# Optimization experiments

Hardware: AMD Instinct MI355X
Metric: run time of the kernel (lower is better)

Reference implementation:

```python
import jax, jax.numpy as jnp
import numpy as np

N_NODES = 50000

def _gat_layer(x, src, dst, W, a_l, a_r, bias, alpha, agg, act, n_nodes):
    # x: [N, in]; W: [in, H*F]; a_l, a_r: [H, F]; bias: [H*F]
    H, F = a_l.shape
    z = (x @ W).reshape(n_nodes, H, F)                      # [N,H,F]
    el = jnp.einsum('nhf,hf->nh', z, a_l)                   # [N,H]
    er = jnp.einsum('nhf,hf->nh', z, a_r)                   # [N,H]
    e = jax.nn.leaky_relu(el[src] + er[dst], alpha)         # [E,H]
    # segment softmax over in-edges of each destination node
    m = jax.ops.segment_max(e, dst, num_segments=n_nodes)   # [N,H]
    ex = jnp.exp(e - m[dst])                                # [E,H]
    s = jax.ops.segment_sum(ex, dst, num_segments=n_nodes)  # [N,H]
    attn = ex / jnp.maximum(s[dst], 1e-9)                   # [E,H]
    msg = attn[:, :, None] * z[src]                         # [E,H,F]
    h = jax.ops.segment_sum(msg, dst, num_segments=n_nodes) # [N,H,F]
    # identity residual (in_feats == H*F) as in DGL GATConv
    h = h + x.reshape(n_nodes, -1, F)
    h = h + bias.reshape(1, H, F)
    if agg == 'flatten':
        h = h.reshape(n_nodes, H * F)
    else:  # mean over heads
        h = h.mean(axis=1)
    if act is not None:
        h = act(h)
    return h


def setup_inputs() -> dict:
    key = jax.random.key(0)
    ks = jax.random.split(key, 14)
    N, E, D = N_NODES, 800000, 128
    H, F = 4, 32
    sc_in = 1.0 / np.sqrt(D)
    sc_h = 1.0 / np.sqrt(H * F)
    inp = {
        'feats': jax.random.normal(ks[0], (N, D), jnp.float32),
        'src': jax.random.randint(ks[1], (E,), 0, N),
        'dst': jax.random.randint(ks[2], (E,), 0, N),
        'W1': jax.random.normal(ks[3], (D, H * F), jnp.float32) * sc_in,
        'al1': jax.random.normal(ks[4], (H, F), jnp.float32) * sc_h,
        'ar1': jax.random.normal(ks[5], (H, F), jnp.float32) * sc_h,
        'b1': jnp.zeros((H * F,), jnp.float32),
        'W2': jax.random.normal(ks[6], (H * F, H * F), jnp.float32) * sc_h,
        'al2': jax.random.normal(ks[7], (H, F), jnp.float32) * sc_h,
        'ar2': jax.random.normal(ks[8], (H, F), jnp.float32) * sc_h,
        'b2': jnp.zeros((H * F,), jnp.float32),
        'Wp': jax.random.normal(ks[9], (F, 1), jnp.float32) / np.sqrt(F),
        'bp': jnp.zeros((1,), jnp.float32),
    }
    return inp


def reference(feats, src, dst, W1, al1, ar1, b1, W2, al2, ar2, b2, Wp, bp):
    h = _gat_layer(feats, src, dst, W1, al1, ar1, b1, 0.2, 'flatten', jax.nn.elu, N_NODES)
    h = _gat_layer(h, src, dst, W2, al2, ar2, b2, 0.2, 'mean', None, N_NODES)
    return h @ Wp + bp  # [N, 1]
```

## Files before the change

kernel.cpp:

```cpp
#include <hip/hip_runtime.h>
#include <hip/hip_bf16.h>

#define NN 50000
#define NE 800000
#define HF 128
#define MAXDEG 64

#define OFF_FLAG   0u
#define OFF_FX     3801088u
#define OFF_WC1    16601088u
#define OFF_WC2    16633856u
#define OFF_PAR    16666624u
#define OFF_Z      16668672u
#define OFF_H1     29468672u
#define OFF_EL     42268672u
#define OFF_ER     43068672u
#define OFF_FILL   54000128u
#define OFF_ADJ2   60000000u

typedef __hip_bfloat16 bf16;
typedef unsigned short us16;

#define PREP_RANK_B   3125
#define PREP_FEATS_B  6250
#define PREP_SMALL_B  132
#define PREP_GRID     (PREP_RANK_B + PREP_FEATS_B + PREP_SMALL_B)
#define GEMM_B 782

typedef __attribute__((ext_vector_type(8))) short bf16x8;
typedef __attribute__((ext_vector_type(4))) float f32x4;

__device__ __forceinline__ float us2f(us16 u) {
  union { unsigned int i; float f; } c; c.i = ((unsigned int)u) << 16; return c.f;
}
__device__ __forceinline__ us16 f2us(float f) {
  bf16 h = __float2bfloat16(f);
  union { bf16 h; us16 u; } c; c.h = h; return c.u;
}
__device__ __forceinline__ float blo(unsigned v) {
  union { unsigned i; float f; } c; c.i = v << 16; return c.f;
}
__device__ __forceinline__ float bhi(unsigned v) {
  union { unsigned i; float f; } c; c.i = v & 0xffff0000u; return c.f;
}
__device__ __forceinline__ unsigned pk2(float a, float b) {
  return (unsigned)f2us(a) | ((unsigned)f2us(b) << 16);
}

__device__ __forceinline__ int detect_f32(const us16* __restrict__ u) {
  int t = threadIdx.x;
  int mx = 0;
  for (int i = t; i < 2048; i += 256) {
    int e = (u[i] >> 7) & 0xFF;
    mx = mx > e ? mx : e;
  }
#pragma unroll
  for (int m = 32; m >= 1; m >>= 1) {
    int o = __shfl_xor(mx, m);
    mx = mx > o ? mx : o;
  }
  __shared__ int sred[4];
  if ((t & 63) == 0) sred[t >> 6] = mx;
  __syncthreads();
  int a = sred[0] > sred[1] ? sred[0] : sred[1];
  int b = sred[2] > sred[3] ? sred[2] : sred[3];
  int r = a > b ? a : b;
  return r >= 135;
}

__global__ __launch_bounds__(256) void k_prep(
    const void* __restrict__ feats, us16* __restrict__ fx,
    const void* s0, const void* s1, const void* s2, const void* s3, const void* s4,
    const void* s5, const void* s6, const void* s7, const void* s8, const void* s9,
    us16* d0, us16* d1, us16* d2, us16* d3, us16* d4,
    us16* d5, us16* d6, us16* d7, us16* d8, us16* d9,
    const int* __restrict__ src, const int* __restrict__ dst,
    int* __restrict__ fill, int* __restrict__ adj2, int* __restrict__ flag) {
  int b = blockIdx.x;
  if (b < PREP_RANK_B) {
    int e = b * 256 + threadIdx.x;
    if (e < NE) {
      int d = dst[e];
      int r = atomicAdd(&fill[d], 1);
      if (r < MAXDEG) adj2[(d << 6) + r] = src[e];
    }
    return;
  }
  int f = detect_f32((const us16*)s0);
  if (b == PREP_RANK_B && threadIdx.x == 0) *flag = f;
  if (b < PREP_RANK_B + PREP_FEATS_B) {
    int i = ((b - PREP_RANK_B) * 256 + threadIdx.x) * 4;
    if (f) {
      float4 v = *(const float4*)((const float*)feats + i);
      ushort4 o;
      o.x = f2us(v.x); o.y = f2us(v.y); o.z = f2us(v.z); o.w = f2us(v.w);
      *(ushort4*)(fx + i) = o;
    } else {
      *(ushort4*)(fx + i) = *(const ushort4*)((const us16*)feats + i);
    }
  } else {
    const void* sp[10] = {s0, s1, s2, s3, s4, s5, s6, s7, s8, s9};
    us16* dp[10] = {d0, d1, d2, d3, d4, d5, d6, d7, d8, d9};
    const int cnt[10] = {16384, 16384, 128, 128, 128, 128, 128, 128, 32, 1};
    int gid = (b - PREP_RANK_B - PREP_FEATS_B) * 256 + threadIdx.x;
    int base = 0;
#pragma unroll
    for (int p = 0; p < 10; ++p) {
      int loc = gid - base;
      if (loc >= 0 && loc < cnt[p])
        dp[p][loc] = f ? f2us(((const float*)sp[p])[loc]) : ((const us16*)sp[p])[loc];
      base += cnt[p];
    }
  }
}

__global__ __launch_bounds__(256) void k_gemm(const us16* __restrict__ X,
                                              const us16* __restrict__ W,
                                              us16* __restrict__ Z,
                                              const us16* __restrict__ al,
                                              const us16* __restrict__ ar,
                                              float* __restrict__ el,
                                              float* __restrict__ er) {
  __shared__ us16 Wl[HF * HF];
  int tid = threadIdx.x;
  for (int e = tid; e < HF * HF; e += 256) {
    int k = e >> 7, n = e & 127;
    int d = ((((k >> 5) * 8 + (n >> 4)) * 4 + ((k >> 3) & 3)) * 16 + (n & 15)) * 8 + (k & 7);
    Wl[d] = W[e];
  }
  __syncthreads();

  int w = tid >> 6;
  int lane = tid & 63;
  int q = lane >> 4;
  int c = lane & 15;
  int m0 = blockIdx.x * 64 + w * 16;

  int rA = m0 + c;
  if (rA >= NN) rA = NN - 1;
  const us16* xrow = X + (size_t)rA * HF;

  f32x4 acc[8] = {};
#pragma unroll
  for (int s = 0; s < 4; ++s) {
    bf16x8 a = *(const bf16x8*)&xrow[s * 32 + q * 8];
#pragma unroll
    for (int t = 0; t < 8; ++t) {
      bf16x8 bb = *(const bf16x8*)&Wl[((((s * 8) + t) * 4 + q) * 16 + c) * 8];
      acc[t] = __builtin_amdgcn_mfma_f32_16x16x32_bf16(a, bb, acc[t], 0, 0, 0);
    }
  }

#pragma unroll
  for (int reg = 0; reg < 4; ++reg) {
    int row = m0 + q * 4 + reg;
    if (row < NN) {
      us16* zrow = Z + (size_t)row * HF;
#pragma unroll
      for (int t = 0; t < 8; ++t) zrow[t * 16 + c] = f2us(acc[t][reg]);
    }
  }

  float alv[8], arv[8];
#pragma unroll
  for (int t = 0; t < 8; ++t) {
    alv[t] = us2f(al[t * 16 + c]);
    arv[t] = us2f(ar[t * 16 + c]);
  }
#pragma unroll
  for (int reg = 0; reg < 4; ++reg) {
    int row = m0 + q * 4 + reg;
    float pl[4], pr[4];
#pragma unroll
    for (int h = 0; h < 4; ++h) {
      pl[h] = acc[2 * h][reg] * alv[2 * h] + acc[2 * h + 1][reg] * alv[2 * h + 1];
      pr[h] = acc[2 * h][reg] * arv[2 * h] + acc[2 * h + 1][reg] * arv[2 * h + 1];
    }
#pragma unroll
    for (int m = 1; m < 16; m <<= 1) {
#pragma unroll
      for (int h = 0; h < 4; ++h) {
        pl[h] += __shfl_xor(pl[h], m);
        pr[h] += __shfl_xor(pr[h], m);
      }
    }
    if (row < NN) {
      int cc = c & 3;
      float vl = cc == 0 ? pl[0] : cc == 1 ? pl[1] : cc == 2 ? pl[2] : pl[3];
      float vr = cc == 0 ? pr[0] : cc == 1 ? pr[1] : cc == 2 ? pr[2] : pr[3];
      if (c < 4) el[row * 4 + cc] = vl;
      else if (c < 8) er[row * 4 + cc] = vr;
    }
  }
}

template <int LAYER>
__global__ __launch_bounds__(256) void k_agg(
    const us16* __restrict__ Z, const float* __restrict__ el,
    const float* __restrict__ er, const int* __restrict__ fill,
    const int* __restrict__ adj2, const us16* __restrict__ resid,
    const us16* __restrict__ bias, us16* __restrict__ Hout,
    const us16* __restrict__ Wp, const us16* __restrict__ bp,
    void* __restrict__ out, const int* __restrict__ flag) {
  int n = blockIdx.x * 4 + (threadIdx.x >> 6);
  int lane = threadIdx.x & 63;
  int g = lane >> 4;
  int p = lane & 15;
  int hl = p >> 2;
  int f0 = p * 8;
  int deg = fill[n];
  if (deg > MAXDEG) deg = MAXDEG;
  int begin = n << 6;
  float erh = er[n * 4 + hl];

  float acc[8] = {};
  float ssum = 0.f;
  int i = g;
  for (; i + 4 < deg; i += 8) {
    int s0 = adj2[begin + i];
    int s1 = adj2[begin + i + 4];
    float l0 = el[s0 * 4 + hl];
    float l1 = el[s1 * 4 + hl];
    uint4 za = *(const uint4*)&Z[(size_t)s0 * HF + f0];
    uint4 zb = *(const uint4*)&Z[(size_t)s1 * HF + f0];
    float sc0 = l0 + erh; sc0 = sc0 > 0.f ? sc0 : 0.2f * sc0;
    float sc1 = l1 + erh; sc1 = sc1 > 0.f ? sc1 : 0.2f * sc1;
    float ex0 = __expf(sc0);
    float ex1 = __expf(sc1);
    ssum += ex0 + ex1;
    acc[0] = fmaf(ex0, blo(za.x), acc[0]); acc[1] = fmaf(ex0, bhi(za.x), acc[1]);
    acc[2] = fmaf(ex0, blo(za.y), acc[2]); acc[3] = fmaf(ex0, bhi(za.y), acc[3]);
    acc[4] = fmaf(ex0, blo(za.z), acc[4]); acc[5] = fmaf(ex0, bhi(za.z), acc[5]);
    acc[6] = fmaf(ex0, blo(za.w), acc[6]); acc[7] = fmaf(ex0, bhi(za.w), acc[7]);
    acc[0] = fmaf(ex1, blo(zb.x), acc[0]); acc[1] = fmaf(ex1, bhi(zb.x), acc[1]);
    acc[2] = fmaf(ex1, blo(zb.y), acc[2]); acc[3] = fmaf(ex1, bhi(zb.y), acc[3]);
    acc[4] = fmaf(ex1, blo(zb.z), acc[4]); acc[5] = fmaf(ex1, bhi(zb.z), acc[5]);
    acc[6] = fmaf(ex1, blo(zb.w), acc[6]); acc[7] = fmaf(ex1, bhi(zb.w), acc[7]);
  }
  if (i < deg) {
    int s = adj2[begin + i];
    float sc = el[s * 4 + hl] + erh;
    sc = sc > 0.f ? sc : 0.2f * sc;
    float ex = __expf(sc);
    ssum += ex;
    uint4 zq = *(const uint4*)&Z[(size_t)s * HF + f0];
    acc[0] = fmaf(ex, blo(zq.x), acc[0]); acc[1] = fmaf(ex, bhi(zq.x), acc[1]);
    acc[2] = fmaf(ex, blo(zq.y), acc[2]); acc[3] = fmaf(ex, bhi(zq.y), acc[3]);
    acc[4] = fmaf(ex, blo(zq.z), acc[4]); acc[5] = fmaf(ex, bhi(zq.z), acc[5]);
    acc[6] = fmaf(ex, blo(zq.w), acc[6]); acc[7] = fmaf(ex, bhi(zq.w), acc[7]);
  }
  ssum += __shfl_xor(ssum, 16); ssum += __shfl_xor(ssum, 32);
#pragma unroll
  for (int j = 0; j < 8; ++j) {
    acc[j] += __shfl_xor(acc[j], 16);
    acc[j] += __shfl_xor(acc[j], 32);
  }
  float inv = 1.f / fmaxf(ssum, 1e-9f);

  uint4 xq = *(const uint4*)&resid[(size_t)n * HF + f0];
  uint4 bq = *(const uint4*)&bias[f0];
  float t0 = fmaf(acc[0], inv, blo(xq.x) + blo(bq.x));
  float t1 = fmaf(acc[1], inv, bhi(xq.x) + bhi(bq.x));
  float t2 = fmaf(acc[2], inv, blo(xq.y) + blo(bq.y));
  float t3 = fmaf(acc[3], inv, bhi(xq.y) + bhi(bq.y));
  float t4 = fmaf(acc[4], inv, blo(xq.z) + blo(bq.z));
  float t5 = fmaf(acc[5], inv, bhi(xq.z) + bhi(bq.z));
  float t6 = fmaf(acc[6], inv, blo(xq.w) + blo(bq.w));
  float t7 = fmaf(acc[7], inv, bhi(xq.w) + bhi(bq.w));

  if (LAYER == 1) {
    t0 = t0 > 0.f ? t0 : __expf(t0) - 1.f;
    t1 = t1 > 0.f ? t1 : __expf(t1) - 1.f;
    t2 = t2 > 0.f ? t2 : __expf(t2) - 1.f;
    t3 = t3 > 0.f ? t3 : __expf(t3) - 1.f;
    t4 = t4 > 0.f ? t4 : __expf(t4) - 1.f;
    t5 = t5 > 0.f ? t5 : __expf(t5) - 1.f;
    t6 = t6 > 0.f ? t6 : __expf(t6) - 1.f;
    t7 = t7 > 0.f ? t7 : __expf(t7) - 1.f;
    if (g == 0) {
      uint4 o;
      o.x = pk2(t0, t1); o.y = pk2(t2, t3); o.z = pk2(t4, t5); o.w = pk2(t6, t7);
      *(uint4*)&Hout[(size_t)n * HF + f0] = o;
    }
  } else {
    t0 += __shfl_xor(t0, 4); t0 += __shfl_xor(t0, 8);
    t1 += __shfl_xor(t1, 4); t1 += __shfl_xor(t1, 8);
    t2 += __shfl_xor(t2, 4); t2 += __shfl_xor(t2, 8);
    t3 += __shfl_xor(t3, 4); t3 += __shfl_xor(t3, 8);
    t4 += __shfl_xor(t4, 4); t4 += __shfl_xor(t4, 8);
    t5 += __shfl_xor(t5, 4); t5 += __shfl_xor(t5, 8);
    t6 += __shfl_xor(t6, 4); t6 += __shfl_xor(t6, 8);
    t7 += __shfl_xor(t7, 4); t7 += __shfl_xor(t7, 8);
    int fw = (p & 3) * 8;
    float pr = 0.25f * (t0 * us2f(Wp[fw]) + t1 * us2f(Wp[fw + 1]) +
                        t2 * us2f(Wp[fw + 2]) + t3 * us2f(Wp[fw + 3]) +
                        t4 * us2f(Wp[fw + 4]) + t5 * us2f(Wp[fw + 5]) +
                        t6 * us2f(Wp[fw + 6]) + t7 * us2f(Wp[fw + 7]));
    pr += __shfl_xor(pr, 1); pr += __shfl_xor(pr, 2);
    if (lane == 0) {
      float res = pr + us2f(bp[0]);
      if (*flag) ((float*)out)[n] = res;
      else ((us16*)out)[n] = f2us(res);
    }
  }
}

extern "C" void kernel_launch(void* const* d_in, const int* in_sizes, int n_in,
                              void* d_out, int out_size, void* d_ws, size_t ws_size,
                              hipStream_t stream) {
  const int* src = (const int*)d_in[1];
  const int* dst = (const int*)d_in[2];
  char* ws = (char*)d_ws;
  int* flag   = (int*)(ws + OFF_FLAG);
  us16* fx    = (us16*)(ws + OFF_FX);
  us16* wc1   = (us16*)(ws + OFF_WC1);
  us16* wc2   = (us16*)(ws + OFF_WC2);
  us16* al1   = (us16*)(ws + OFF_PAR + 0);
  us16* ar1   = (us16*)(ws + OFF_PAR + 256);
  us16* b1    = (us16*)(ws + OFF_PAR + 512);
  us16* al2   = (us16*)(ws + OFF_PAR + 768);
  us16* ar2   = (us16*)(ws + OFF_PAR + 1024);
  us16* b2    = (us16*)(ws + OFF_PAR + 1280);
  us16* wp    = (us16*)(ws + OFF_PAR + 1536);
  us16* bp    = (us16*)(ws + OFF_PAR + 1792);
  us16* z     = (us16*)(ws + OFF_Z);
  us16* h1    = (us16*)(ws + OFF_H1);
  float* el   = (float*)(ws + OFF_EL);
  float* er   = (float*)(ws + OFF_ER);
  int* fill   = (int*)(ws + OFF_FILL);
  int* adj2   = (int*)(ws + OFF_ADJ2);

  hipMemsetAsync(fill, 0, (size_t)NN * 4, stream);

  hipLaunchKernelGGL(k_prep, dim3(PREP_GRID), dim3(256), 0, stream,
                     d_in[0], fx,
                     d_in[3], d_in[7], d_in[4], d_in[5], d_in[6],
                     d_in[8], d_in[9], d_in[10], d_in[11], d_in[12],
                     wc1, wc2, al1, ar1, b1, al2, ar2, b2, wp, bp,
                     src, dst, fill, adj2, flag);

  hipLaunchKernelGGL(k_gemm, dim3(GEMM_B), dim3(256), 0, stream, fx, wc1, z,
                     al1, ar1, el, er);
  hipLaunchKernelGGL((k_agg<1>), dim3(NN / 4), dim3(256), 0, stream, z, el, er, fill, adj2,
                     fx, b1, h1, (us16*)nullptr, (us16*)nullptr, (void*)nullptr, flag);
  hipLaunchKernelGGL(k_gemm, dim3(GEMM_B), dim3(256), 0, stream, h1, wc2, z,
                     al2, ar2, el, er);
  hipLaunchKernelGGL((k_agg<2>), dim3(NN / 4), dim3(256), 0, stream, z, el, er, fill, adj2,
                     h1, b2, (us16*)nullptr, wp, bp, d_out, flag);
}
```

Baseline: 241.6 us.

## Fuse input conversion and adjacency scatter into layer-1 GEMM kernel

Removes the separate prep kernel that converted features and parameters to bf16 in workspace. The layer-1 GEMM now also hosts the edge-scatter blocks and converts fp32 inputs on the fly, and the aggregation kernels read residual, bias and projection weights directly in their native dtype. This cuts one launch and a full read/write pass over the feature matrix, at the cost of more branching and wider fp32 loads in the GEMM and aggregation kernels.

```diff
diff --git a/kernel.cpp b/kernel.cpp
--- a/kernel.cpp
+++ b/kernel.cpp
@@ -7,10 +7,6 @@
 #define MAXDEG 64
 
 #define OFF_FLAG   0u
-#define OFF_FX     3801088u
-#define OFF_WC1    16601088u
-#define OFF_WC2    16633856u
-#define OFF_PAR    16666624u
 #define OFF_Z      16668672u
 #define OFF_H1     29468672u
 #define OFF_EL     42268672u
@@ -21,10 +17,7 @@
 typedef __hip_bfloat16 bf16;
 typedef unsigned short us16;
 
-#define PREP_RANK_B   3125
-#define PREP_FEATS_B  6250
-#define PREP_SMALL_B  132
-#define PREP_GRID     (PREP_RANK_B + PREP_FEATS_B + PREP_SMALL_B)
+#define SCAT_B 3125
 #define GEMM_B 782
 
 typedef __attribute__((ext_vector_type(8))) short bf16x8;
@@ -68,65 +61,42 @@
   return r >= 135;
 }
 
-__global__ __launch_bounds__(256) void k_prep(
-    const void* __restrict__ feats, us16* __restrict__ fx,
-    const void* s0, const void* s1, const void* s2, const void* s3, const void* s4,
-    const void* s5, const void* s6, const void* s7, const void* s8, const void* s9,
-    us16* d0, us16* d1, us16* d2, us16* d3, us16* d4,
-    us16* d5, us16* d6, us16* d7, us16* d8, us16* d9,
+template <int LAYER>
+__global__ __launch_bounds__(256) void k_gemm(
+    const void* __restrict__ Xv, const void* __restrict__ Wv,
+    const void* __restrict__ alr, const void* __restrict__ arr,
+    us16* __restrict__ Z, float* __restrict__ el, float* __restrict__ er,
     const int* __restrict__ src, const int* __restrict__ dst,
-    int* __restrict__ fill, int* __restrict__ adj2, int* __restrict__ flag) {
-  int b = blockIdx.x;
-  if (b < PREP_RANK_B) {
-    int e = b * 256 + threadIdx.x;
-    if (e < NE) {
+    int* __restrict__ fill, int* __restrict__ adj2, int* __restrict__ flagp) {
+  if (LAYER == 1) {
+    if ((int)blockIdx.x < SCAT_B) {
+      int e = blockIdx.x * 256 + threadIdx.x;
       int d = dst[e];
       int r = atomicAdd(&fill[d], 1);
       if (r < MAXDEG) adj2[(d << 6) + r] = src[e];
-    }
-    return;
-  }
-  int f = detect_f32((const us16*)s0);
-  if (b == PREP_RANK_B && threadIdx.x == 0) *flag = f;
-  if (b < PREP_RANK_B + PREP_FEATS_B) {
-    int i = ((b - PREP_RANK_B) * 256 + threadIdx.x) * 4;
-    if (f) {
-      float4 v = *(const float4*)((const float*)feats + i);
-      ushort4 o;
-      o.x = f2us(v.x); o.y = f2us(v.y); o.z = f2us(v.z); o.w = f2us(v.w);
-      *(ushort4*)(fx + i) = o;
-    } else {
-      *(ushort4*)(fx + i) = *(const ushort4*)((const us16*)feats + i);
-    }
+      return;
+    }
+  }
+  int bx = (LAYER == 1) ? (int)blockIdx.x - SCAT_B : (int)blockIdx.x;
+
+  __shared__ us16 Wl[HF * HF];
+  int f;
+  if (LAYER == 1) {
+    f = detect_f32((const us16*)Wv);
+    if (bx == 0 && threadIdx.x == 0) *flagp = f;
   } else {
-    const void* sp[10] = {s0, s1, s2, s3, s4, s5, s6, s7, s8, s9};
-    us16* dp[10] = {d0, d1, d2, d3, d4, d5, d6, d7, d8, d9};
-    const int cnt[10] = {16384, 16384, 128, 128, 128, 128, 128, 128, 32, 1};
-    int gid = (b - PREP_RANK_B - PREP_FEATS_B) * 256 + threadIdx.x;
-    int base = 0;
-#pragma unroll
-    for (int p = 0; p < 10; ++p) {
-      int loc = gid - base;
-      if (loc >= 0 && loc < cnt[p])
-        dp[p][loc] = f ? f2us(((const float*)sp[p])[loc]) : ((const us16*)sp[p])[loc];
-      base += cnt[p];
-    }
-  }
-}
-
-__global__ __launch_bounds__(256) void k_gemm(const us16* __restrict__ X,
-                                              const us16* __restrict__ W,
-                                              us16* __restrict__ Z,
-                                              const us16* __restrict__ al,
-                                              const us16* __restrict__ ar,
-                                              float* __restrict__ el,
-                                              float* __restrict__ er) {
-  __shared__ us16 Wl[HF * HF];
+    f = *flagp;
+  }
+
   int tid = threadIdx.x;
-  for (int e = tid; e < HF * HF; e += 256) {
-    int k = e >> 7, n = e & 127;
-    int d = ((((k >> 5) * 8 + (n >> 4)) * 4 + ((k >> 3) & 3)) * 16 + (n & 15)) * 8 + (k & 7);
-    Wl[d] = W[e];
+  {
+    const float* Wf = (const float*)Wv;
+    const us16* Wb = (const us16*)Wv;
+    for (int e = tid; e < HF * HF; e += 256) {
+      int k = e >> 7, n = e & 127;
+      int d = ((((k >> 5) * 8 + (n >> 4)) * 4 + ((k >> 3) & 3)) * 16 + (n & 15)) * 8 + (k & 7);
+      Wl[d] = f ? f2us(Wf[e]) : Wb[e];
+    }
   }
   __syncthreads();
 
@@ -134,16 +104,29 @@
   int lane = tid & 63;
   int q = lane >> 4;
   int c = lane & 15;
-  int m0 = blockIdx.x * 64 + w * 16;
+  int m0 = bx * 64 + w * 16;
 
   int rA = m0 + c;
   if (rA >= NN) rA = NN - 1;
-  const us16* xrow = X + (size_t)rA * HF;
+  const us16* xb = (const us16*)Xv + (size_t)rA * HF;
+  const float* xf = (const float*)Xv + (size_t)rA * HF;
 
   f32x4 acc[8] = {};
 #pragma unroll
   for (int s = 0; s < 4; ++s) {
-    bf16x8 a = *(const bf16x8*)&xrow[s * 32 + q * 8];
+    bf16x8 a;
+    if (LAYER == 1 && f) {
+      float4 v0 = *(const float4*)&xf[s * 32 + q * 8];
+      float4 v1 = *(const float4*)&xf[s * 32 + q * 8 + 4];
+      union { us16 u[8]; bf16x8 v; } cv;
+      cv.u[0] = f2us(v0.x); cv.u[1] = f2us(v0.y);
+      cv.u[2] = f2us(v0.z); cv.u[3] = f2us(v0.w);
+      cv.u[4] = f2us(v1.x); cv.u[5] = f2us(v1.y);
+      cv.u[6] = f2us(v1.z); cv.u[7] = f2us(v1.w);
+      a = cv.v;
+    } else {
+      a = *(const bf16x8*)&xb[s * 32 + q * 8];
+    }
 #pragma unroll
     for (int t = 0; t < 8; ++t) {
       bf16x8 bb = *(const bf16x8*)&Wl[((((s * 8) + t) * 4 + q) * 16 + c) * 8];
@@ -162,10 +145,14 @@
   }
 
   float alv[8], arv[8];
-#pragma unroll
-  for (int t = 0; t < 8; ++t) {
-    alv[t] = us2f(al[t * 16 + c]);
-    arv[t] = us2f(ar[t * 16 + c]);
+  {
+    const float* alf = (const float*)alr; const us16* alb = (const us16*)alr;
+    const float* arf = (const float*)arr; const us16* arb = (const us16*)arr;
+#pragma unroll
+    for (int t = 0; t < 8; ++t) {
+      alv[t] = f ? alf[t * 16 + c] : us2f(alb[t * 16 + c]);
+      arv[t] = f ? arf[t * 16 + c] : us2f(arb[t * 16 + c]);
+    }
   }
 #pragma unroll
   for (int reg = 0; reg < 4; ++reg) {
@@ -198,10 +185,11 @@
 __global__ __launch_bounds__(256) void k_agg(
     const us16* __restrict__ Z, const float* __restrict__ el,
     const float* __restrict__ er, const int* __restrict__ fill,
-    const int* __restrict__ adj2, const us16* __restrict__ resid,
-    const us16* __restrict__ bias, us16* __restrict__ Hout,
-    const us16* __restrict__ Wp, const us16* __restrict__ bp,
+    const int* __restrict__ adj2, const void* __restrict__ resid,
+    const void* __restrict__ bias, us16* __restrict__ Hout,
+    const void* __restrict__ Wp, const void* __restrict__ bp,
     void* __restrict__ out, const int* __restrict__ flag) {
+  int f = *flag;
   int n = blockIdx.x * 4 + (threadIdx.x >> 6);
   int lane = threadIdx.x & 63;
   int g = lane >> 4;
@@ -257,16 +245,36 @@
   }
   float inv = 1.f / fmaxf(ssum, 1e-9f);
 
-  uint4 xq = *(const uint4*)&resid[(size_t)n * HF + f0];
-  uint4 bq = *(const uint4*)&bias[f0];
-  float t0 = fmaf(acc[0], inv, blo(xq.x) + blo(bq.x));
-  float t1 = fmaf(acc[1], inv, bhi(xq.x) + bhi(bq.x));
-  float t2 = fmaf(acc[2], inv, blo(xq.y) + blo(bq.y));
-  float t3 = fmaf(acc[3], inv, bhi(xq.y) + bhi(bq.y));
-  float t4 = fmaf(acc[4], inv, blo(xq.z) + blo(bq.z));
-  float t5 = fmaf(acc[5], inv, bhi(xq.z) + bhi(bq.z));
-  float t6 = fmaf(acc[6], inv, blo(xq.w) + blo(bq.w));
-  float t7 = fmaf(acc[7], inv, bhi(xq.w) + bhi(bq.w));
+  float rx[8];
+  if (LAYER == 1 && f) {
+    const float* rf = (const float*)resid + (size_t)n * HF + f0;
+    float4 r0 = *(const float4*)rf;
+    float4 r1 = *(const float4*)(rf + 4);
+    rx[0] = r0.x; rx[1] = r0.y; rx[2] = r0.z; rx[3] = r0.w;
+    rx[4] = r1.x; rx[5] = r1.y; rx[6] = r1.z; rx[7] = r1.w;
+  } else {
+    uint4 xq = *(const uint4*)((const us16*)resid + (size_t)n * HF + f0);
+    rx[0] = blo(xq.x); rx[1] = bhi(xq.x); rx[2] = blo(xq.y); rx[3] = bhi(xq.y);
+    rx[4] = blo(xq.z); rx[5] = bhi(xq.z); rx[6] = blo(xq.w); rx[7] = bhi(xq.w);
+  }
+  float bv[8];
+  if (f) {
+    const float* bf_ = (const float*)bias + f0;
+    bv[0] = bf_[0]; bv[1] = bf_[1]; bv[2] = bf_[2]; bv[3] = bf_[3];
+    bv[4] = bf_[4]; bv[5] = bf_[5]; bv[6] = bf_[6]; bv[7] = bf_[7];
+  } else {
+    uint4 bq = *(const uint4*)((const us16*)bias + f0);
+    bv[0] = blo(bq.x); bv[1] = bhi(bq.x); bv[2] = blo(bq.y); bv[3] = bhi(bq.y);
+    bv[4] = blo(bq.z); bv[5] = bhi(bq.z); bv[6] = blo(bq.w); bv[7] = bhi(bq.w);
+  }
+  float t0 = fmaf(acc[0], inv, rx[0] + bv[0]);
+  float t1 = fmaf(acc[1], inv, rx[1] + bv[1]);
+  float t2 = fmaf(acc[2], inv, rx[2] + bv[2]);
+  float t3 = fmaf(acc[3], inv, rx[3] + bv[3]);
+  float t4 = fmaf(acc[4], inv, rx[4] + bv[4]);
+  float t5 = fmaf(acc[5], inv, rx[5] + bv[5]);
+  float t6 = fmaf(acc[6], inv, rx[6] + bv[6]);
+  float t7 = fmaf(acc[7], inv, rx[7] + bv[7]);
 
   if (LAYER == 1) {
     t0 = t0 > 0.f ? t0 : __expf(t0) - 1.f;
@@ -292,14 +300,25 @@
     t6 += __shfl_xor(t6, 4); t6 += __shfl_xor(t6, 8);
     t7 += __shfl_xor(t7, 4); t7 += __shfl_xor(t7, 8);
     int fw = (p & 3) * 8;
-    float pr = 0.25f * (t0 * us2f(Wp[fw]) + t1 * us2f(Wp[fw + 1]) +
-                        t2 * us2f(Wp[fw + 2]) + t3 * us2f(Wp[fw + 3]) +
-                        t4 * us2f(Wp[fw + 4]) + t5 * us2f(Wp[fw + 5]) +
-                        t6 * us2f(Wp[fw + 6]) + t7 * us2f(Wp[fw + 7]));
+    float wv0, wv1, wv2, wv3, wv4, wv5, wv6, wv7;
+    if (f) {
+      const float* wpf = (const float*)Wp;
+      wv0 = wpf[fw];     wv1 = wpf[fw + 1]; wv2 = wpf[fw + 2]; wv3 = wpf[fw + 3];
+      wv4 = wpf[fw + 4]; wv5 = wpf[fw + 5]; wv6 = wpf[fw + 6]; wv7 = wpf[fw + 7];
+    } else {
+      const us16* wpb = (const us16*)Wp;
+      wv0 = us2f(wpb[fw]);     wv1 = us2f(wpb[fw + 1]);
+      wv2 = us2f(wpb[fw + 2]); wv3 = us2f(wpb[fw + 3]);
+      wv4 = us2f(wpb[fw + 4]); wv5 = us2f(wpb[fw + 5]);
+      wv6 = us2f(wpb[fw + 6]); wv7 = us2f(wpb[fw + 7]);
+    }
+    float pr = 0.25f * (t0 * wv0 + t1 * wv1 + t2 * wv2 + t3 * wv3 +
+                        t4 * wv4 + t5 * wv5 + t6 * wv6 + t7 * wv7);
     pr += __shfl_xor(pr, 1); pr += __shfl_xor(pr, 2);
     if (lane == 0) {
-      float res = pr + us2f(bp[0]);
-      if (*flag) ((float*)out)[n] = res;
+      float bpv = f ? ((const float*)bp)[0] : us2f(((const us16*)bp)[0]);
+      float res = pr + bpv;
+      if (f) ((float*)out)[n] = res;
       else ((us16*)out)[n] = f2us(res);
     }
   }
@@ -312,17 +331,6 @@
   const int* dst = (const int*)d_in[2];
   char* ws = (char*)d_ws;
   int* flag   = (int*)(ws + OFF_FLAG);
-  us16* fx    = (us16*)(ws + OFF_FX);
-  us16* wc1   = (us16*)(ws + OFF_WC1);
-  us16* wc2   = (us16*)(ws + OFF_WC2);
-  us16* al1   = (us16*)(ws + OFF_PAR + 0);
-  us16* ar1   = (us16*)(ws + OFF_PAR + 256);
-  us16* b1    = (us16*)(ws + OFF_PAR + 512);
-  us16* al2   = (us16*)(ws + OFF_PAR + 768);
-  us16* ar2   = (us16*)(ws + OFF_PAR + 1024);
-  us16* b2    = (us16*)(ws + OFF_PAR + 1280);
-  us16* wp    = (us16*)(ws + OFF_PAR + 1536);
-  us16* bp    = (us16*)(ws + OFF_PAR + 1792);
   us16* z     = (us16*)(ws + OFF_Z);
   us16* h1    = (us16*)(ws + OFF_H1);
   float* el   = (float*)(ws + OFF_EL);
@@ -332,19 +340,16 @@
 
   hipMemsetAsync(fill, 0, (size_t)NN * 4, stream);
 
-  hipLaunchKernelGGL(k_prep, dim3(PREP_GRID), dim3(256), 0, stream,
-                     d_in[0], fx,
-                     d_in[3], d_in[7], d_in[4], d_in[5], d_in[6],
-                     d_in[8], d_in[9], d_in[10], d_in[11], d_in[12],
-                     wc1, wc2, al1, ar1, b1, al2, ar2, b2, wp, bp,
+  hipLaunchKernelGGL((k_gemm<1>), dim3(SCAT_B + GEMM_B), dim3(256), 0, stream,
+                     d_in[0], d_in[3], d_in[4], d_in[5], z, el, er,
                      src, dst, fill, adj2, flag);
-
-  hipLaunchKernelGGL(k_gemm, dim3(GEMM_B), dim3(256), 0, stream, fx, wc1, z,
-                     al1, ar1, el, er);
-  hipLaunchKernelGGL((k_agg<1>), dim3(NN / 4), dim3(256), 0, stream, z, el, er, fill, adj2,
-                     fx, b1, h1, (us16*)nullptr, (us16*)nullptr, (void*)nullptr, flag);
-  hipLaunchKernelGGL(k_gemm, dim3(GEMM_B), dim3(256), 0, stream, h1, wc2, z,
-                     al2, ar2, el, er);
-  hipLaunchKernelGGL((k_agg<2>), dim3(NN / 4), dim3(256), 0, stream, z, el, er, fill, adj2,
-                     h1, b2, (us16*)nullptr, wp, bp, d_out, flag);
-}
+  hipLaunchKernelGGL((k_agg<1>), dim3(NN / 4), dim3(256), 0, stream, z, el, er,
+                     fill, adj2, d_in[0], d_in[6], h1,
+                     (const void*)nullptr, (const void*)nullptr, (void*)nullptr, flag);
+  hipLaunchKernelGGL((k_gemm<2>), dim3(GEMM_B), dim3(256), 0, stream,
+                     h1, d_in[7], d_in[8], d_in[9], z, el, er,
+                     src, dst, fill, adj2, flag);
+  hipLaunchKernelGGL((k_agg<2>), dim3(NN / 4), dim3(256), 0, stream, z, el, er,
+                     fill, adj2, h1, d_in[10], (us16*)nullptr,
+                     d_in[11], d_in[12], d_out, flag);
+}
```

Result: slower. 283.0 us (+17.1%).

## Store adjacency as 16-bit indices and pre-swizzle GEMM weights in prep

Applied to the files above, without the earlier changes.

The prep kernel now writes the weight matrices already in the MFMA-friendly swizzled layout. The GEMM kernel therefore drops its per-block LDS staging and __syncthreads and reads B fragments straight from global memory (L2-resident), with A fragments hoisted into registers. Separately, the padded adjacency list is stored as uint16 instead of int32, which halves the index traffic in both aggregation kernels. This relies on node ids fitting in 16 bits (NN=50000), and it trades LDS reuse of the weights for repeated global/L2 loads per wave.

```diff
diff --git a/kernel.cpp b/kernel.cpp
--- a/kernel.cpp
+++ b/kernel.cpp
@@ -75,14 +75,14 @@
     us16* d0, us16* d1, us16* d2, us16* d3, us16* d4,
     us16* d5, us16* d6, us16* d7, us16* d8, us16* d9,
     const int* __restrict__ src, const int* __restrict__ dst,
-    int* __restrict__ fill, int* __restrict__ adj2, int* __restrict__ flag) {
+    int* __restrict__ fill, us16* __restrict__ adj2, int* __restrict__ flag) {
   int b = blockIdx.x;
   if (b < PREP_RANK_B) {
     int e = b * 256 + threadIdx.x;
     if (e < NE) {
       int d = dst[e];
       int r = atomicAdd(&fill[d], 1);
-      if (r < MAXDEG) adj2[(d << 6) + r] = src[e];
+      if (r < MAXDEG) adj2[(d << 6) + r] = (us16)src[e];
     }
     return;
   }
@@ -107,29 +107,29 @@
 #pragma unroll
     for (int p = 0; p < 10; ++p) {
       int loc = gid - base;
-      if (loc >= 0 && loc < cnt[p])
-        dp[p][loc] = f ? f2us(((const float*)sp[p])[loc]) : ((const us16*)sp[p])[loc];
+      if (loc >= 0 && loc < cnt[p]) {
+        us16 v = f ? f2us(((const float*)sp[p])[loc]) : ((const us16*)sp[p])[loc];
+        if (p < 2) {
+          int k = loc >> 7, n = loc & 127;
+          int d = ((((k >> 5) * 8 + (n >> 4)) * 4 + ((k >> 3) & 3)) * 16 + (n & 15)) * 8 + (k & 7);
+          dp[p][d] = v;
+        } else {
+          dp[p][loc] = v;
+        }
+      }
       base += cnt[p];
     }
   }
 }
 
 __global__ __launch_bounds__(256) void k_gemm(const us16* __restrict__ X,
-                                              const us16* __restrict__ W,
+                                              const us16* __restrict__ Wc,
                                               us16* __restrict__ Z,
                                               const us16* __restrict__ al,
                                               const us16* __restrict__ ar,
                                               float* __restrict__ el,
                                               float* __restrict__ er) {
-  __shared__ us16 Wl[HF * HF];
   int tid = threadIdx.x;
-  for (int e = tid; e < HF * HF; e += 256) {
-    int k = e >> 7, n = e & 127;
-    int d = ((((k >> 5) * 8 + (n >> 4)) * 4 + ((k >> 3) & 3)) * 16 + (n & 15)) * 8 + (k & 7);
-    Wl[d] = W[e];
-  }
-  __syncthreads();
-
   int w = tid >> 6;
   int lane = tid & 63;
   int q = lane >> 4;
@@ -140,14 +140,17 @@
   if (rA >= NN) rA = NN - 1;
   const us16* xrow = X + (size_t)rA * HF;
 
+  bf16x8 afr[4];
+#pragma unroll
+  for (int s = 0; s < 4; ++s) afr[s] = *(const bf16x8*)&xrow[s * 32 + q * 8];
+
   f32x4 acc[8] = {};
-#pragma unroll
+#pragma unroll 1
   for (int s = 0; s < 4; ++s) {
-    bf16x8 a = *(const bf16x8*)&xrow[s * 32 + q * 8];
 #pragma unroll
     for (int t = 0; t < 8; ++t) {
-      bf16x8 bb = *(const bf16x8*)&Wl[((((s * 8) + t) * 4 + q) * 16 + c) * 8];
-      acc[t] = __builtin_amdgcn_mfma_f32_16x16x32_bf16(a, bb, acc[t], 0, 0, 0);
+      bf16x8 bb = *(const bf16x8*)&Wc[(size_t)((s * 8 + t) * 64 + lane) * 8];
+      acc[t] = __builtin_amdgcn_mfma_f32_16x16x32_bf16(afr[s], bb, acc[t], 0, 0, 0);
     }
   }
 
@@ -198,7 +201,7 @@
 __global__ __launch_bounds__(256) void k_agg(
     const us16* __restrict__ Z, const float* __restrict__ el,
     const float* __restrict__ er, const int* __restrict__ fill,
-    const int* __restrict__ adj2, const us16* __restrict__ resid,
+    const us16* __restrict__ adj2, const us16* __restrict__ resid,
     const us16* __restrict__ bias, us16* __restrict__ Hout,
     const us16* __restrict__ Wp, const us16* __restrict__ bp,
     void* __restrict__ out, const int* __restrict__ flag) {
@@ -217,8 +220,8 @@
   float ssum = 0.f;
   int i = g;
   for (; i + 4 < deg; i += 8) {
-    int s0 = adj2[begin + i];
-    int s1 = adj2[begin + i + 4];
+    int s0 = (int)adj2[begin + i];
+    int s1 = (int)adj2[begin + i + 4];
     float l0 = el[s0 * 4 + hl];
     float l1 = el[s1 * 4 + hl];
     uint4 za = *(const uint4*)&Z[(size_t)s0 * HF + f0];
@@ -238,7 +241,7 @@
     acc[6] = fmaf(ex1, blo(zb.w), acc[6]); acc[7] = fmaf(ex1, bhi(zb.w), acc[7]);
   }
   if (i < deg) {
-    int s = adj2[begin + i];
+    int s = (int)adj2[begin + i];
     float sc = el[s * 4 + hl] + erh;
     sc = sc > 0.f ? sc : 0.2f * sc;
     float ex = __expf(sc);
@@ -328,7 +331,7 @@
   float* el   = (float*)(ws + OFF_EL);
   float* er   = (float*)(ws + OFF_ER);
   int* fill   = (int*)(ws + OFF_FILL);
-  int* adj2   = (int*)(ws + OFF_ADJ2);
+  us16* adj2  = (us16*)(ws + OFF_ADJ2);
 
   hipMemsetAsync(fill, 0, (size_t)NN * 4, stream);
 
@@ -341,10 +344,12 @@
 
   hipLaunchKernelGGL(k_gemm, dim3(GEMM_B), dim3(256), 0, stream, fx, wc1, z,
                      al1, ar1, el, er);
-  hipLaunchKernelGGL((k_agg<1>), dim3(NN / 4), dim3(256), 0, stream, z, el, er, fill, adj2,
-                     fx, b1, h1, (us16*)nullptr, (us16*)nullptr, (void*)nullptr, flag);
+  hipLaunchKernelGGL((k_agg<1>), dim3(NN / 4), dim3(256), 0, stream, z, el, er,
+                     fill, adj2, fx, b1, h1,
+                     (const us16*)nullptr, (const us16*)nullptr, (void*)nullptr, flag);
   hipLaunchKernelGGL(k_gemm, dim3(GEMM_B), dim3(256), 0, stream, h1, wc2, z,
                      al2, ar2, el, er);
-  hipLaunchKernelGGL((k_agg<2>), dim3(NN / 4), dim3(256), 0, stream, z, el, er, fill, adj2,
-                     h1, b2, (us16*)nullptr, wp, bp, d_out, flag);
-}
+  hipLaunchKernelGGL((k_agg<2>), dim3(NN / 4), dim3(256), 0, stream, z, el, er,
+                     fill, adj2, h1, b2, (us16*)nullptr,
+                     wp, bp, d_out, flag);
+}
```

New measurement: 282.0 us. 16.7% more time.
